# Kernel optimization log

Measured on AMD Instinct MI355X. Metric: run time of the kernel, lower is better.

The kernel has to match this reference:

```python
import jax, jax.numpy as jnp
import numpy as np

D_K = 1  # global d_k from the source module


def setup_inputs() -> dict:
    key = jax.random.key(0)
    kq, kk, kv = jax.random.split(key, 3)
    B, H, S, Dv = 8, 8, 16384, 64
    Q = jax.random.normal(kq, (B, H, S, 1), dtype=jnp.float32)
    K = jax.random.normal(kk, (B, H, S, 1), dtype=jnp.float32)
    V = jax.random.normal(kv, (B, H, S, Dv), dtype=jnp.float32)
    return {"Q": Q, "K": K, "V": V}


def reference(Q, K, V):
    # Frobenius norm over the sequence axis (dim=2), unsqueezed at dim 3
    # K, Q: [B, H, S, 1] -> norm: [B, H, 1] -> [B, H, 1, 1]
    Kn = jnp.expand_dims(jnp.sqrt(jnp.sum(K * K, axis=2)), axis=3)
    Qn = jnp.expand_dims(jnp.sqrt(jnp.sum(Q * Q, axis=2)), axis=3)
    K = K / Kn
    Q = Q / Qn
    # Linear-attention reorder: (K^T V) first -> [B, H, 1, Dv]
    K_TV = jnp.einsum("bhsd,bhse->bhde", K, V) / np.float32(np.sqrt(D_K))
    # Q @ (K^T V) -> [B, H, S, Dv]
    context = jnp.einsum("bhsd,bhde->bhse", Q, K_TV)
    return context
```

## Files before the change

### kernel.cpp

```cpp
#include <hip/hip_runtime.h>
#include <math.h>

#define S_LEN 16384
#define DV    64
#define NBH   64
#define NBLK  16
#define CHUNK (S_LEN / NBLK)


__global__ __launch_bounds__(256) void stage1_partial_ktv(
    const float* __restrict__ K, const float* __restrict__ V,
    float* __restrict__ partial) {
    const int bh  = blockIdx.x >> 4;
    const int blk = blockIdx.x & 15;
    const int tid = threadIdx.x;
    const int e4  = tid & 15;
    const int sg  = tid >> 4;

    const float*  Kb = K + (size_t)bh * S_LEN;
    const float4* Vb = (const float4*)(V + (size_t)bh * S_LEN * DV);

    const int s0 = blk * CHUNK;
    float4 acc = make_float4(0.f, 0.f, 0.f, 0.f);
    #pragma unroll 4
    for (int i = 0; i < CHUNK / 16; ++i) {
        const int s = s0 + i * 16 + sg;
        const float  k = Kb[s];
        const float4 v = Vb[(size_t)s * 16 + e4];
        acc.x += k * v.x; acc.y += k * v.y;
        acc.z += k * v.z; acc.w += k * v.w;
    }

    __shared__ float4 red[16][16];
    red[sg][e4] = acc;
    __syncthreads();

    if (tid < DV) {
        const float* base = (const float*)red;
        float s = 0.f;
        #pragma unroll
        for (int p = 0; p < 16; ++p) s += base[p * DV + tid];
        partial[((size_t)bh * NBLK + blk) * DV + tid] = s;
    }
}

__global__ __launch_bounds__(256) void stage2_finalize(
    const float* __restrict__ Q, const float* __restrict__ K,
    const float* __restrict__ partial, float* __restrict__ fk) {
    const int bh  = blockIdx.x;
    const int tid = threadIdx.x;

    const float4* Q4 = (const float4*)(Q + (size_t)bh * S_LEN);
    const float4* K4 = (const float4*)(K + (size_t)bh * S_LEN);

    float qss = 0.f, kss = 0.f;
    for (int i = tid; i < S_LEN / 4; i += 256) {
        const float4 q = Q4[i];
        const float4 k = K4[i];
        qss += q.x * q.x + q.y * q.y + q.z * q.z + q.w * q.w;
        kss += k.x * k.x + k.y * k.y + k.z * k.z + k.w * k.w;
    }

    __shared__ float rq[256], rk[256];
    rq[tid] = qss; rk[tid] = kss;
    __syncthreads();
    #pragma unroll
    for (int off = 128; off > 0; off >>= 1) {
        if (tid < off) { rq[tid] += rq[tid + off]; rk[tid] += rk[tid + off]; }
        __syncthreads();
    }

    __shared__ float inv_norm;
    if (tid == 0) inv_norm = 1.0f / (sqrtf(rq[0]) * sqrtf(rk[0]));
    __syncthreads();

    if (tid < DV) {
        float s = 0.f;
        #pragma unroll
        for (int p = 0; p < NBLK; ++p)
            s += partial[((size_t)bh * NBLK + p) * DV + tid];
        fk[(size_t)bh * DV + tid] = s * inv_norm;
    }
}

__global__ __launch_bounds__(256) void stage3_outer(
    const float* __restrict__ Q, const float* __restrict__ fk,
    float4* __restrict__ out) {
    const size_t idx = (size_t)blockIdx.x * 256 + threadIdx.x;
    const int e4 = (int)(idx & 15);
    const int s  = (int)((idx >> 4) & (S_LEN - 1));
    const int bh = (int)(idx >> 18);

    const float  q = Q[(size_t)bh * S_LEN + s];
    const float4 f = ((const float4*)fk)[(size_t)bh * 16 + e4];
    out[idx] = make_float4(q * f.x, q * f.y, q * f.z, q * f.w);
}

extern "C" void kernel_launch(void* const* d_in, const int* in_sizes, int n_in,
                              void* d_out, int out_size, void* d_ws, size_t ws_size,
                              hipStream_t stream) {
    const float* Q = (const float*)d_in[0];
    const float* K = (const float*)d_in[1];
    const float* V = (const float*)d_in[2];
    float* out = (float*)d_out;

    float* partial = (float*)d_ws;
    float* fk      = partial + (size_t)NBH * NBLK * DV;

    stage1_partial_ktv<<<NBH * NBLK, 256, 0, stream>>>(K, V, partial);
    stage2_finalize<<<NBH, 256, 0, stream>>>(Q, K, partial, fk);

    const int n4 = NBH * S_LEN * (DV / 4);
    stage3_outer<<<n4 / 256, 256, 0, stream>>>(Q, fk, (float4*)out);
}
```

Before: 461.8 us.

## Fuse norm reductions into stage1, use nontemporal loads/stores and persistent output loop

Moves the Q and K sum-of-squares reductions into the first kernel, where each block also handles a chunk of the sequence. Per-block partial norms are written out, so the finalize kernel becomes a tiny 64-thread reduction and no longer rescans Q and K. V loads and output stores use nontemporal builtins to avoid polluting the cache with streaming data. The output kernel now runs 2048 blocks, each looping over 32 rows and loading fk once, instead of launching one thread per float4. The work is dominated by the 256MB V read and 256MB output write, so the gain is limited mostly to launch and cache effects.

```diff
diff --git a/kernel.cpp b/kernel.cpp
--- a/kernel.cpp
+++ b/kernel.cpp
@@ -7,32 +7,47 @@
 #define NBLK  16
 #define CHUNK (S_LEN / NBLK)
 
+typedef float vf4 __attribute__((ext_vector_type(4)));
 
-__global__ __launch_bounds__(256) void stage1_partial_ktv(
-    const float* __restrict__ K, const float* __restrict__ V,
-    float* __restrict__ partial) {
+
+__global__ __launch_bounds__(256) void stage1_partial(
+    const float* __restrict__ Q, const float* __restrict__ K,
+    const float* __restrict__ V,
+    float* __restrict__ pktv, float* __restrict__ pqk) {
     const int bh  = blockIdx.x >> 4;
     const int blk = blockIdx.x & 15;
     const int tid = threadIdx.x;
     const int e4  = tid & 15;
     const int sg  = tid >> 4;
 
-    const float*  Kb = K + (size_t)bh * S_LEN;
-    const float4* Vb = (const float4*)(V + (size_t)bh * S_LEN * DV);
+    const float* Kb = K + (size_t)bh * S_LEN + blk * CHUNK;
+    const float* Qb = Q + (size_t)bh * S_LEN + blk * CHUNK;
+    const vf4*   Vb = (const vf4*)(V + (size_t)bh * S_LEN * DV)
+                      + (size_t)blk * CHUNK * (DV / 4);
 
-    const int s0 = blk * CHUNK;
-    float4 acc = make_float4(0.f, 0.f, 0.f, 0.f);
+    vf4 acc = {0.f, 0.f, 0.f, 0.f};
     #pragma unroll 4
     for (int i = 0; i < CHUNK / 16; ++i) {
-        const int s = s0 + i * 16 + sg;
-        const float  k = Kb[s];
-        const float4 v = Vb[(size_t)s * 16 + e4];
-        acc.x += k * v.x; acc.y += k * v.y;
-        acc.z += k * v.z; acc.w += k * v.w;
+        const int s = i * 16 + sg;
+        const float k = Kb[s];
+        const vf4 v = __builtin_nontemporal_load(Vb + s * (DV / 4) + e4);
+        acc += k * v;
     }
 
-    __shared__ float4 red[16][16];
+    const vf4 q4 = ((const vf4*)Qb)[tid];
+    const vf4 k4 = ((const vf4*)Kb)[tid];
+    float qss = q4.x * q4.x + q4.y * q4.y + q4.z * q4.z + q4.w * q4.w;
+    float kss = k4.x * k4.x + k4.y * k4.y + k4.z * k4.z + k4.w * k4.w;
+    #pragma unroll
+    for (int off = 32; off > 0; off >>= 1) {
+        qss += __shfl_down(qss, off);
+        kss += __shfl_down(kss, off);
+    }
+
+    __shared__ vf4 red[16][16];
+    __shared__ float rq[4], rk[4];
     red[sg][e4] = acc;
+    if ((tid & 63) == 0) { rq[tid >> 6] = qss; rk[tid >> 6] = kss; }
     __syncthreads();
 
     if (tid < DV) {
@@ -40,60 +55,59 @@
         float s = 0.f;
         #pragma unroll
         for (int p = 0; p < 16; ++p) s += base[p * DV + tid];
-        partial[((size_t)bh * NBLK + blk) * DV + tid] = s;
+        pktv[((size_t)bh * NBLK + blk) * DV + tid] = s;
+    }
+    if (tid == 0) {
+        pqk[(bh * NBLK + blk) * 2 + 0] = rq[0] + rq[1] + rq[2] + rq[3];
+        pqk[(bh * NBLK + blk) * 2 + 1] = rk[0] + rk[1] + rk[2] + rk[3];
     }
 }
 
-__global__ __launch_bounds__(256) void stage2_finalize(
-    const float* __restrict__ Q, const float* __restrict__ K,
-    const float* __restrict__ partial, float* __restrict__ fk) {
+__global__ __launch_bounds__(64) void stage2_finalize(
+    const float* __restrict__ pktv, const float* __restrict__ pqk,
+    float* __restrict__ fk) {
     const int bh  = blockIdx.x;
     const int tid = threadIdx.x;
 
-    const float4* Q4 = (const float4*)(Q + (size_t)bh * S_LEN);
-    const float4* K4 = (const float4*)(K + (size_t)bh * S_LEN);
+    float qss = 0.f, kss = 0.f;
+    if (tid < NBLK) {
+        qss = pqk[(bh * NBLK + tid) * 2 + 0];
+        kss = pqk[(bh * NBLK + tid) * 2 + 1];
+    }
+    #pragma unroll
+    for (int off = 8; off > 0; off >>= 1) {
+        qss += __shfl_down(qss, off);
+        kss += __shfl_down(kss, off);
+    }
+    const float inv = 1.0f / (sqrtf(__shfl(qss, 0)) * sqrtf(__shfl(kss, 0)));
 
-    float qss = 0.f, kss = 0.f;
-    for (int i = tid; i < S_LEN / 4; i += 256) {
-        const float4 q = Q4[i];
-        const float4 k = K4[i];
-        qss += q.x * q.x + q.y * q.y + q.z * q.z + q.w * q.w;
-        kss += k.x * k.x + k.y * k.y + k.z * k.z + k.w * k.w;
-    }
+    float s = 0.f;
+    #pragma unroll
+    for (int p = 0; p < NBLK; ++p)
+        s += pktv[((size_t)bh * NBLK + p) * DV + tid];
+    fk[bh * DV + tid] = s * inv;
+}
 
-    __shared__ float rq[256], rk[256];
-    rq[tid] = qss; rk[tid] = kss;
-    __syncthreads();
-    #pragma unroll
-    for (int off = 128; off > 0; off >>= 1) {
-        if (tid < off) { rq[tid] += rq[tid + off]; rk[tid] += rk[tid + off]; }
-        __syncthreads();
-    }
-
-    __shared__ float inv_norm;
-    if (tid == 0) inv_norm = 1.0f / (sqrtf(rq[0]) * sqrtf(rk[0]));
-    __syncthreads();
-
-    if (tid < DV) {
-        float s = 0.f;
-        #pragma unroll
-        for (int p = 0; p < NBLK; ++p)
-            s += partial[((size_t)bh * NBLK + p) * DV + tid];
-        fk[(size_t)bh * DV + tid] = s * inv_norm;
-    }
-}
+#define S3_BLOCKS 2048
+#define F4_TOTAL  (NBH * S_LEN * (DV / 4))
+#define F4_PER_BLOCK (F4_TOTAL / S3_BLOCKS)
 
 __global__ __launch_bounds__(256) void stage3_outer(
     const float* __restrict__ Q, const float* __restrict__ fk,
-    float4* __restrict__ out) {
-    const size_t idx = (size_t)blockIdx.x * 256 + threadIdx.x;
-    const int e4 = (int)(idx & 15);
-    const int s  = (int)((idx >> 4) & (S_LEN - 1));
-    const int bh = (int)(idx >> 18);
+    vf4* __restrict__ out) {
+    const size_t base = (size_t)blockIdx.x * F4_PER_BLOCK;
+    const int tid = threadIdx.x;
+    const int bh  = (int)(base >> 18);
+    const int e4  = tid & 15;
+    const vf4 f = ((const vf4*)fk)[bh * 16 + e4];
+    const float* Qb = Q + (size_t)bh * S_LEN;
+    const int s0 = (int)((base >> 4) & (S_LEN - 1)) + (tid >> 4);
 
-    const float  q = Q[(size_t)bh * S_LEN + s];
-    const float4 f = ((const float4*)fk)[(size_t)bh * 16 + e4];
-    out[idx] = make_float4(q * f.x, q * f.y, q * f.z, q * f.w);
+    #pragma unroll 8
+    for (int t = 0; t < 32; ++t) {
+        const float q = Qb[s0 + t * 16];
+        __builtin_nontemporal_store(q * f, out + base + t * 256 + tid);
+    }
 }
 
 extern "C" void kernel_launch(void* const* d_in, const int* in_sizes, int n_in,
@@ -104,12 +118,11 @@
     const float* V = (const float*)d_in[2];
     float* out = (float*)d_out;
 
-    float* partial = (float*)d_ws;
-    float* fk      = partial + (size_t)NBH * NBLK * DV;
+    float* pktv = (float*)d_ws;
+    float* pqk  = pktv + (size_t)NBH * NBLK * DV;
+    float* fk   = pqk + NBH * NBLK * 2;
 
-    stage1_partial_ktv<<<NBH * NBLK, 256, 0, stream>>>(K, V, partial);
-    stage2_finalize<<<NBH, 256, 0, stream>>>(Q, K, partial, fk);
-
-    const int n4 = NBH * S_LEN * (DV / 4);
-    stage3_outer<<<n4 / 256, 256, 0, stream>>>(Q, fk, (float4*)out);
+    stage1_partial<<<NBH * NBLK, 256, 0, stream>>>(Q, K, V, pktv, pqk);
+    stage2_finalize<<<NBH, 64, 0, stream>>>(pktv, pqk, fk);
+    stage3_outer<<<S3_BLOCKS, 256, 0, stream>>>(Q, fk, (vf4*)out);
 }
```

Result: faster. 436.0 us (-5.6%).
